# Kernel tuning notes

Hardware: AMD Instinct MI355X
Metric: run time of the kernel (lower is better)

The kernel has to match this reference:

```python
import jax, jax.numpy as jnp
import numpy as np

NUM_EMB = 8192
DIM = 64
DECAY = 0.99
EPS = 1e-05
COMMIT = 0.25


def setup_inputs() -> dict:
    key = jax.random.key(0)
    k1, k2, k3 = jax.random.split(key, 3)
    inputs = jax.random.normal(k1, (8, 4096, DIM), jnp.float32)
    weight = jax.random.normal(k2, (NUM_EMB, DIM), jnp.float32)
    ema_cluster_count = jnp.ones((NUM_EMB,), jnp.float32)
    ema_weight_sum = jax.random.normal(k3, (NUM_EMB, DIM), jnp.float32)
    return {
        'inputs': inputs,
        'weight': weight,
        'ema_cluster_count': ema_cluster_count,
        'ema_weight_sum': ema_weight_sum,
    }


def reference(inputs, weight, ema_cluster_count, ema_weight_sum):
    flat = inputs.reshape(-1, DIM)  # [N, D]
    distances = (
        jnp.sum(flat ** 2, axis=1, keepdims=True)
        + jnp.sum(weight ** 2, axis=1)
        - 2.0 * flat @ weight.T
    )
    idx = jnp.argmin(distances, axis=1)  # [N] int

    # EMA stats (training branch): one-hot column sums == segment counts,
    # encodings.T @ flat == segment sums of inputs by code index.
    counts = jax.ops.segment_sum(
        jnp.ones(flat.shape[0], jnp.float32), idx, num_segments=NUM_EMB)
    new_cc = ema_cluster_count * DECAY + (1.0 - DECAY) * counts
    emb_sum = jax.ops.segment_sum(flat, idx, num_segments=NUM_EMB)
    new_ws = ema_weight_sum * DECAY + (1.0 - DECAY) * emb_sum

    n = jnp.sum(new_cc)
    smoothed = (new_cc + EPS) / (n + NUM_EMB * EPS) * n
    new_weight = new_ws / smoothed[:, None]  # updated codebook [K, D]

    quantized_raw = new_weight[idx].reshape(inputs.shape)
    e_latent_loss = jnp.mean((jax.lax.stop_gradient(quantized_raw) - inputs) ** 2)
    vq_loss = COMMIT * e_latent_loss

    avg_probs = counts / flat.shape[0]
    perplexity = jnp.exp(-jnp.sum(avg_probs * jnp.log(avg_probs + 1e-10)))

    # straight-through estimator
    quantized = inputs + jax.lax.stop_gradient(quantized_raw - inputs)
    return quantized, vq_loss, idx, perplexity, new_weight, new_cc, new_ws
```

## Files before the change

kernel.cpp:

```cpp
#include <hip/hip_runtime.h>
#include <math.h>

typedef _Float16 f16x8 __attribute__((ext_vector_type(8)));
typedef float f32x4 __attribute__((ext_vector_type(4)));

#define NROWS 32768
#define KEMB  8192

#define DECAYF 0.99f
#define OMDF   0.01f

#define OUT_Q    0
#define OUT_LOSS 2097152
#define OUT_IDX  2097153
#define OUT_PERP 2129921
#define OUT_NW   2129922
#define OUT_NCC  2654210
#define OUT_NWS  2662402

#define WS_N      0
#define WS_ENT    1
#define WS_COUNTS 4
#define WS_EMB    8196
#define WS_IDX    532484
#define WS_W2H    565252
#define WS_WFRAG  573444
#define WS_ZERO_UNITS 532484

__device__ __forceinline__ float sq_rn(float v) { return __fmul_rn(v, v); }

__device__ __forceinline__ float npsumsq64(const float* vbuf) {
  float a[8];
#pragma unroll
  for (int j = 0; j < 8; ++j) a[j] = sq_rn(vbuf[j]);
#pragma unroll
  for (int m = 1; m < 8; ++m)
#pragma unroll
    for (int j = 0; j < 8; ++j) a[j] = __fadd_rn(a[j], sq_rn(vbuf[m*8 + j]));
  return __fadd_rn(__fadd_rn(__fadd_rn(a[0],a[1]), __fadd_rn(a[2],a[3])),
                   __fadd_rn(__fadd_rn(a[4],a[5]), __fadd_rn(a[6],a[7])));
}

__device__ __forceinline__ void split_f16(float x, _Float16& hi, _Float16& lo) {
  hi = (_Float16)x;
  float r = __fsub_rn(x, (float)hi);
  lo = (_Float16)r;
}

__global__ __launch_bounds__(256) void prep_kernel(const float* __restrict__ wg,
                                                   float* __restrict__ ws) {
  const int tid = blockIdx.x * 256 + threadIdx.x;
  if (tid < KEMB) {
    const float* src = wg + (size_t)tid * 64;
    float vbuf[64];
#pragma unroll
    for (int f = 0; f < 16; ++f) {
      float4 v = *(const float4*)(src + f*4);
      vbuf[f*4+0]=v.x; vbuf[f*4+1]=v.y; vbuf[f*4+2]=v.z; vbuf[f*4+3]=v.w;
    }
    ws[WS_W2H + tid] = __fmul_rn(0.5f, npsumsq64(vbuf));
  } else if (tid < KEMB + 65536) {
    const int u = tid - KEMB;
    const int K = u >> 3, g = u & 7;
    const int n = K & 15, P = K >> 4;
    const int slot = (g&3)*16 + n, shi = g >> 2;
    const float* src = wg + (size_t)K*64 + g*8;
    float4 v0 = *(const float4*)src, v1 = *(const float4*)(src + 4);
    float vv[8] = {v0.x,v0.y,v0.z,v0.w,v1.x,v1.y,v1.z,v1.w};
    f16x8 hi, lo;
#pragma unroll
    for (int j = 0; j < 8; ++j) { _Float16 h, l; split_f16(vv[j], h, l); hi[j]=h; lo[j]=l; }
    _Float16* wf = (_Float16*)(ws + WS_WFRAG);
    *(f16x8*)&wf[((size_t)(P*4 + shi)*64 + slot)*8]     = hi;
    *(f16x8*)&wf[((size_t)(P*4 + 2 + shi)*64 + slot)*8] = lo;
  }
}

#define LOADP(H0, H1, L0, L1, CW, WP, CP)           \
  H0 = *(const f16x8*)(WP);                         \
  H1 = *(const f16x8*)(WP + 512);                   \
  L0 = *(const f16x8*)(WP + 1024);                  \
  L1 = *(const f16x8*)(WP + 1536);                  \
  CW = *(const f32x4*)(CP);                         \
  WP += 16384; CP += 128;

#define TOURN(ACC, C0)                                                       \
  _Pragma("unroll")                                                          \
  for (int bt = 0; bt < 4; ++bt) {                                           \
    const float d0 = ACC[bt][0], d1 = ACC[bt][1], d2 = ACC[bt][2], d3 = ACC[bt][3]; \
    const float m01 = fminf(d0, d1), m23 = fminf(d2, d3);                    \
    const float pm  = fminf(m01, m23);                                       \
    const int i01 = (d1 < d0) ? 1 : 0;                                       \
    const int i23 = (d3 < d2) ? 3 : 2;                                       \
    const int isel = (m23 < m01) ? i23 : i01;                                \
    if (pm < bestd[bt]) { bestd[bt] = pm; bestk[bt] = (C0) + isel; }         \
  }

__global__ __attribute__((amdgpu_flat_work_group_size(256,256), amdgpu_waves_per_eu(2,2)))
void argmin_kernel(const float* __restrict__ xg,
                   float* __restrict__ out,
                   float* __restrict__ ws) {
  __shared__ __align__(16) _Float16 xp[4*4*64*8];
  __shared__ float md[64*4];
  __shared__ int   mk[64*4];
  __shared__ int   bkL[64];

  const int t    = threadIdx.x;
  const int lane = t & 63, wv = t >> 6;
  const int quad = lane >> 4, n16 = lane & 15;
  const int cg = wv;
  const int row0 = blockIdx.x * 64;
  const _Float16* __restrict__ wfrag = (const _Float16*)(ws + WS_WFRAG);
  const float* __restrict__ w2hg = ws + WS_W2H;

#pragma unroll
  for (int it = 0; it < 2; ++it) {
    const int u  = t + 256*it;
    const int rp = u >> 7, n = (u >> 3) & 15, g = u & 7;
    const float* src = xg + (size_t)(row0 + rp*16 + n)*64 + g*8;
    float4 v0 = *(const float4*)src, v1 = *(const float4*)(src + 4);
    float vv[8] = {v0.x,v0.y,v0.z,v0.w,v1.x,v1.y,v1.z,v1.w};
    f16x8 hi, lo;
#pragma unroll
    for (int j = 0; j < 8; ++j) { _Float16 h, l; split_f16(-vv[j], h, l); hi[j]=h; lo[j]=l; }
    const int slot = (g&3)*16 + n, shi = g >> 2;
    *(f16x8*)&xp[(((rp*4) + shi)*64 + slot)*8]     = hi;
    *(f16x8*)&xp[(((rp*4) + 2 + shi)*64 + slot)*8] = lo;
  }
  __syncthreads();

  f16x8 b[4][4];
#pragma unroll
  for (int bt = 0; bt < 4; ++bt)
#pragma unroll
    for (int s = 0; s < 4; ++s)
      b[bt][s] = *(const f16x8*)&xp[(((bt*4) + s)*64 + lane)*8];

  float bestd[4]; int bestk[4];
#pragma unroll
  for (int i = 0; i < 4; ++i) { bestd[i] = INFINITY; bestk[i] = 0; }

  const int q4 = quad * 4;

  const _Float16* wpA = wfrag + (size_t)cg * 2048 + (size_t)lane * 8;
  const _Float16* wpB = wpA + 8192;
  const float*    cpA = w2hg + cg*16 + q4;
  const float*    cpB = cpA + 64;

  f16x8 hA0, hA1, lA0, lA1, hB0, hB1, lB0, lB1;
  f32x4 cwA, cwB;

  LOADP(hA0, hA1, lA0, lA1, cwA, wpA, cpA);
  LOADP(hB0, hB1, lB0, lB1, cwB, wpB, cpB);

  f32x4 accA[4], accB[4];
  int c0A = cg*16 + q4;
  int c0B = c0A + 64;

#pragma unroll 1
  for (int j = 0; j < 64; ++j) {
    __builtin_amdgcn_s_setprio(1);
#pragma unroll
    for (int bt = 0; bt < 4; ++bt) accA[bt] = __builtin_amdgcn_mfma_f32_16x16x32_f16(hA0, b[bt][0], cwA,      0,0,0);
#pragma unroll
    for (int bt = 0; bt < 4; ++bt) accB[bt] = __builtin_amdgcn_mfma_f32_16x16x32_f16(hB0, b[bt][0], cwB,      0,0,0);
#pragma unroll
    for (int bt = 0; bt < 4; ++bt) accA[bt] = __builtin_amdgcn_mfma_f32_16x16x32_f16(hA1, b[bt][1], accA[bt], 0,0,0);
#pragma unroll
    for (int bt = 0; bt < 4; ++bt) accB[bt] = __builtin_amdgcn_mfma_f32_16x16x32_f16(hB1, b[bt][1], accB[bt], 0,0,0);
#pragma unroll
    for (int bt = 0; bt < 4; ++bt) accA[bt] = __builtin_amdgcn_mfma_f32_16x16x32_f16(hA0, b[bt][2], accA[bt], 0,0,0);
#pragma unroll
    for (int bt = 0; bt < 4; ++bt) accB[bt] = __builtin_amdgcn_mfma_f32_16x16x32_f16(hB0, b[bt][2], accB[bt], 0,0,0);
#pragma unroll
    for (int bt = 0; bt < 4; ++bt) accA[bt] = __builtin_amdgcn_mfma_f32_16x16x32_f16(hA1, b[bt][3], accA[bt], 0,0,0);
#pragma unroll
    for (int bt = 0; bt < 4; ++bt) accB[bt] = __builtin_amdgcn_mfma_f32_16x16x32_f16(hB1, b[bt][3], accB[bt], 0,0,0);
#pragma unroll
    for (int bt = 0; bt < 4; ++bt) accA[bt] = __builtin_amdgcn_mfma_f32_16x16x32_f16(lA0, b[bt][0], accA[bt], 0,0,0);
#pragma unroll
    for (int bt = 0; bt < 4; ++bt) accB[bt] = __builtin_amdgcn_mfma_f32_16x16x32_f16(lB0, b[bt][0], accB[bt], 0,0,0);
#pragma unroll
    for (int bt = 0; bt < 4; ++bt) accA[bt] = __builtin_amdgcn_mfma_f32_16x16x32_f16(lA1, b[bt][1], accA[bt], 0,0,0);
#pragma unroll
    for (int bt = 0; bt < 4; ++bt) accB[bt] = __builtin_amdgcn_mfma_f32_16x16x32_f16(lB1, b[bt][1], accB[bt], 0,0,0);
    __builtin_amdgcn_s_setprio(0);

    if (j < 63) {
      LOADP(hA0, hA1, lA0, lA1, cwA, wpA, cpA);
      LOADP(hB0, hB1, lB0, lB1, cwB, wpB, cpB);
    }

    TOURN(accA, c0A);
    c0A += 128;
    TOURN(accB, c0B);
    c0B += 128;
  }

#pragma unroll
  for (int bt = 0; bt < 4; ++bt) {
    float bd = bestd[bt]; int bk = bestk[bt];
#pragma unroll
    for (int m = 16; m < 64; m <<= 1) {
      const float od = __shfl_xor(bd, m, 64);
      const int   ok = __shfl_xor(bk, m, 64);
      if (od < bd || (od == bd && ok < bk)) { bd = od; bk = ok; }
    }
    if (lane < 16) {
      const int row = bt*16 + n16;
      md[row*4 + cg] = bd;
      mk[row*4 + cg] = bk;
    }
  }
  __syncthreads();

  if (t < 64) {
    const int row = t;
    float bd = md[row*4]; int bk = mk[row*4];
#pragma unroll
    for (int u2 = 1; u2 < 4; ++u2) {
      const float d2 = md[row*4 + u2]; const int k2 = mk[row*4 + u2];
      if (d2 < bd || (d2 == bd && k2 < bk)) { bd = d2; bk = k2; }
    }
    out[OUT_IDX + row0 + row] = (float)bk;
    ((int*)ws)[WS_IDX + row0 + row] = bk;
    bkL[row] = bk;
    atomicAdd(&ws[WS_COUNTS + bk], 1.0f);
  }
  __syncthreads();

#pragma unroll 4
  for (int r = 0; r < 16; ++r) {
    const int row = wv*16 + r;
    const int k = bkL[row];
    atomicAdd(&ws[WS_EMB + (size_t)k*64 + lane],
              xg[(size_t)(row0 + row)*64 + lane]);
  }
}

__global__ __launch_bounds__(256) void stats_kernel(const float* __restrict__ cc,
                                                    float* __restrict__ out,
                                                    float* __restrict__ ws) {
  const int t = threadIdx.x;
  float v1 = 0.0f, v2 = 0.0f;
#pragma unroll
  for (int i = 0; i < 32; ++i) {
    const int k = i*256 + t;
    const float cnt = ws[WS_COUNTS + k];
    const float ncc = __fadd_rn(__fmul_rn(DECAYF, cc[k]), __fmul_rn(OMDF, cnt));
    out[OUT_NCC + k] = ncc;
    const float p = cnt * (1.0f/32768.0f);
    v1 += ncc;
    v2 += __fmul_rn(p, logf(__fadd_rn(p, 1e-10f)));
  }
#pragma unroll
  for (int off = 32; off > 0; off >>= 1) {
    v1 += __shfl_down(v1, off);
    v2 += __shfl_down(v2, off);
  }
  __shared__ float s1[4], s2[4];
  const int lane = t & 63, wid = t >> 6;
  if (lane == 0) { s1[wid] = v1; s2[wid] = v2; }
  __syncthreads();
  if (t == 0) {
    ws[WS_N]   = (s1[0]+s1[1]) + (s1[2]+s1[3]);
    ws[WS_ENT] = (s2[0]+s2[1]) + (s2[2]+s2[3]);
  }
}

__global__ __launch_bounds__(256) void update_quant_kernel(const float* __restrict__ xg,
                                                           const float* __restrict__ ws0,
                                                           float* __restrict__ out,
                                                           float* __restrict__ ws) {
  const int t = threadIdx.x;
  const float n = ws[WS_N];
  const float den = __fadd_rn(n, 0.08192f);

  const int e4 = blockIdx.x * 256 + t;
  {
    const int k = e4 >> 4;
    const float ncc = out[OUT_NCC + k];
    const float smoothed = __fmul_rn(__fadd_rn(ncc, 1e-5f) / den, n);
    float4 w0 = *(const float4*)(ws0 + (size_t)e4*4);
    float4 em = *(const float4*)(ws + WS_EMB + (size_t)e4*4);
    float wv4[4] = {w0.x, w0.y, w0.z, w0.w};
    float ev4[4] = {em.x, em.y, em.z, em.w};
    float nwsv[4], nwv[4];
#pragma unroll
    for (int i = 0; i < 4; ++i) {
      nwsv[i] = __fadd_rn(__fmul_rn(DECAYF, wv4[i]), __fmul_rn(OMDF, ev4[i]));
      nwv[i]  = nwsv[i] / smoothed;
    }
    float4 onws = {nwsv[0], nwsv[1], nwsv[2], nwsv[3]};
    float4 onw  = {nwv[0],  nwv[1],  nwv[2],  nwv[3]};
    *(float4*)(out + OUT_NWS + (size_t)e4*4) = onws;
    *(float4*)(out + OUT_NW  + (size_t)e4*4) = onw;
    if (e4 == 0) out[OUT_PERP] = expf(-ws[WS_ENT]);
  }

  const int* idxb = (const int*)ws + WS_IDX;
  float v = 0.0f;
#pragma unroll
  for (int j = 0; j < 4; ++j) {
    const int qe4 = (j*512 + blockIdx.x)*256 + t;
    const int row = qe4 >> 4, d = (qe4 & 15) * 4;
    const int k = idxb[row];
    const float ncc = out[OUT_NCC + k];
    const float smK = __fmul_rn(__fadd_rn(ncc, 1e-5f) / den, n);
    float4 wq = *(const float4*)(ws0 + (size_t)k*64 + d);
    float4 eq = *(const float4*)(ws + WS_EMB + (size_t)k*64 + d);
    float4 x  = *(const float4*)(xg + (size_t)qe4*4);
    float wv4[4] = {wq.x,wq.y,wq.z,wq.w};
    float ev4[4] = {eq.x,eq.y,eq.z,eq.w};
    float xv[4]  = {x.x,x.y,x.z,x.w};
    float4 o; float ov[4];
#pragma unroll
    for (int i = 0; i < 4; ++i) {
      const float nws = __fadd_rn(__fmul_rn(DECAYF, wv4[i]), __fmul_rn(OMDF, ev4[i]));
      const float q = nws / smK;
      const float df = __fsub_rn(q, xv[i]);
      ov[i] = __fadd_rn(xv[i], df);
      v = fmaf(df, df, v);
    }
    o.x = ov[0]; o.y = ov[1]; o.z = ov[2]; o.w = ov[3];
    *(float4*)(out + OUT_Q + (size_t)qe4*4) = o;
  }
#pragma unroll
  for (int off = 32; off > 0; off >>= 1) v += __shfl_down(v, off);
  __shared__ float sm[4];
  const int lane = t & 63, wid = t >> 6;
  if (lane == 0) sm[wid] = v;
  __syncthreads();
  if (t == 0) ws[WS_COUNTS + blockIdx.x] = (sm[0]+sm[1]) + (sm[2]+sm[3]);
}

__global__ void final_kernel(float* __restrict__ out, const float* __restrict__ ws) {
  const int t = threadIdx.x;
  float v = 0.0f;
#pragma unroll
  for (int i = 0; i < 8; ++i) v += ws[WS_COUNTS + i*64 + t];
#pragma unroll
  for (int off = 32; off > 0; off >>= 1) v += __shfl_down(v, off);
  if (t == 0) out[OUT_LOSS] = __fmul_rn(0.25f, v / 2097152.0f);
}

extern "C" void kernel_launch(void* const* d_in, const int* in_sizes, int n_in,
                              void* d_out, int out_size, void* d_ws, size_t ws_size,
                              hipStream_t stream) {
  (void)in_sizes; (void)n_in; (void)out_size; (void)ws_size;
  const float* x   = (const float*)d_in[0];
  const float* w   = (const float*)d_in[1];
  const float* cc  = (const float*)d_in[2];
  const float* ws0 = (const float*)d_in[3];
  float* out = (float*)d_out;
  float* ws  = (float*)d_ws;

  hipMemsetAsync(d_ws, 0, (size_t)WS_ZERO_UNITS * 4, stream);
  hipLaunchKernelGGL(prep_kernel,         dim3(288), dim3(256), 0, stream, w, ws);
  hipLaunchKernelGGL(argmin_kernel,       dim3(512), dim3(256), 0, stream, x, out, ws);
  hipLaunchKernelGGL(stats_kernel,        dim3(1),   dim3(256), 0, stream, cc, out, ws);
  hipLaunchKernelGGL(update_quant_kernel, dim3(512), dim3(256), 0, stream, x, ws0, out, ws);
  hipLaunchKernelGGL(final_kernel,        dim3(1),   dim3(64),  0, stream, out, ws);
}
```

Baseline: 178.5 us.

## Fold memset, stats and final reduction into neighboring kernels via last-block counters

The workspace memset moves into prep_kernel as a grid-stride zeroing loop. The single-block stats kernel and the final loss reduction are folded into the tails of argmin_kernel and update_quant_kernel. A global atomic counter elects the last finishing block to run them, guarded by thread fences. This cuts the launch count from five operations to three and removes the gaps between dependent launches. The cost is extra fences and atomics at the end of each block, plus reliance on the counters being zeroed in prep.

```diff
diff --git a/kernel.cpp b/kernel.cpp
--- a/kernel.cpp
+++ b/kernel.cpp
@@ -20,6 +20,8 @@
 
 #define WS_N      0
 #define WS_ENT    1
+#define WS_CTR    2
+#define WS_CTR2   3
 #define WS_COUNTS 4
 #define WS_EMB    8196
 #define WS_IDX    532484
@@ -50,6 +52,8 @@
 __global__ __launch_bounds__(256) void prep_kernel(const float* __restrict__ wg,
                                                    float* __restrict__ ws) {
   const int tid = blockIdx.x * 256 + threadIdx.x;
+  for (int z = tid; z < WS_ZERO_UNITS; z += 73728) ws[z] = 0.0f;
+
   if (tid < KEMB) {
     const float* src = wg + (size_t)tid * 64;
     float vbuf[64];
@@ -98,12 +102,15 @@
 
 __global__ __attribute__((amdgpu_flat_work_group_size(256,256), amdgpu_waves_per_eu(2,2)))
 void argmin_kernel(const float* __restrict__ xg,
+                   const float* __restrict__ cc,
                    float* __restrict__ out,
                    float* __restrict__ ws) {
   __shared__ __align__(16) _Float16 xp[4*4*64*8];
   __shared__ float md[64*4];
   __shared__ int   mk[64*4];
   __shared__ int   bkL[64];
+  __shared__ float s1[4], s2[4];
+  __shared__ int   amLast;
 
   const int t    = threadIdx.x;
   const int lane = t & 63, wv = t >> 6;
@@ -236,35 +243,34 @@
     atomicAdd(&ws[WS_EMB + (size_t)k*64 + lane],
               xg[(size_t)(row0 + row)*64 + lane]);
   }
-}
-
-__global__ __launch_bounds__(256) void stats_kernel(const float* __restrict__ cc,
-                                                    float* __restrict__ out,
-                                                    float* __restrict__ ws) {
-  const int t = threadIdx.x;
-  float v1 = 0.0f, v2 = 0.0f;
-#pragma unroll
-  for (int i = 0; i < 32; ++i) {
-    const int k = i*256 + t;
-    const float cnt = ws[WS_COUNTS + k];
-    const float ncc = __fadd_rn(__fmul_rn(DECAYF, cc[k]), __fmul_rn(OMDF, cnt));
-    out[OUT_NCC + k] = ncc;
-    const float p = cnt * (1.0f/32768.0f);
-    v1 += ncc;
-    v2 += __fmul_rn(p, logf(__fadd_rn(p, 1e-10f)));
-  }
-#pragma unroll
-  for (int off = 32; off > 0; off >>= 1) {
-    v1 += __shfl_down(v1, off);
-    v2 += __shfl_down(v2, off);
-  }
-  __shared__ float s1[4], s2[4];
-  const int lane = t & 63, wid = t >> 6;
-  if (lane == 0) { s1[wid] = v1; s2[wid] = v2; }
-  __syncthreads();
-  if (t == 0) {
-    ws[WS_N]   = (s1[0]+s1[1]) + (s1[2]+s1[3]);
-    ws[WS_ENT] = (s2[0]+s2[1]) + (s2[2]+s2[3]);
+
+  __threadfence();
+  if (t == 0) amLast = (atomicAdd((int*)ws + WS_CTR, 1) == (int)gridDim.x - 1);
+  __syncthreads();
+  if (amLast) {
+    __threadfence();
+    float v1 = 0.0f, v2 = 0.0f;
+#pragma unroll
+    for (int i = 0; i < 32; ++i) {
+      const int k = i*256 + t;
+      const float cnt = ws[WS_COUNTS + k];
+      const float ncc = __fadd_rn(__fmul_rn(DECAYF, cc[k]), __fmul_rn(OMDF, cnt));
+      out[OUT_NCC + k] = ncc;
+      const float p = cnt * (1.0f/32768.0f);
+      v1 += ncc;
+      v2 += __fmul_rn(p, logf(__fadd_rn(p, 1e-10f)));
+    }
+#pragma unroll
+    for (int off = 32; off > 0; off >>= 1) {
+      v1 += __shfl_down(v1, off);
+      v2 += __shfl_down(v2, off);
+    }
+    if (lane == 0) { s1[wv] = v1; s2[wv] = v2; }
+    __syncthreads();
+    if (t == 0) {
+      ws[WS_N]   = (s1[0]+s1[1]) + (s1[2]+s1[3]);
+      ws[WS_ENT] = (s2[0]+s2[1]) + (s2[2]+s2[3]);
+    }
   }
 }
 
@@ -272,6 +278,8 @@
                                                            const float* __restrict__ ws0,
                                                            float* __restrict__ out,
                                                            float* __restrict__ ws) {
+  __shared__ float sm[4];
+  __shared__ int amL;
   const int t = threadIdx.x;
   const float n = ws[WS_N];
   const float den = __fadd_rn(n, 0.08192f);
@@ -327,21 +335,25 @@
   }
 #pragma unroll
   for (int off = 32; off > 0; off >>= 1) v += __shfl_down(v, off);
-  __shared__ float sm[4];
   const int lane = t & 63, wid = t >> 6;
   if (lane == 0) sm[wid] = v;
   __syncthreads();
   if (t == 0) ws[WS_COUNTS + blockIdx.x] = (sm[0]+sm[1]) + (sm[2]+sm[3]);
-}
-
-__global__ void final_kernel(float* __restrict__ out, const float* __restrict__ ws) {
-  const int t = threadIdx.x;
-  float v = 0.0f;
-#pragma unroll
-  for (int i = 0; i < 8; ++i) v += ws[WS_COUNTS + i*64 + t];
-#pragma unroll
-  for (int off = 32; off > 0; off >>= 1) v += __shfl_down(v, off);
-  if (t == 0) out[OUT_LOSS] = __fmul_rn(0.25f, v / 2097152.0f);
+
+  __threadfence();
+  if (t == 0) amL = (atomicAdd((int*)ws + WS_CTR2, 1) == (int)gridDim.x - 1);
+  __syncthreads();
+  if (amL) {
+    __threadfence();
+    if (t < 64) {
+      float vv = 0.0f;
+#pragma unroll
+      for (int i = 0; i < 8; ++i) vv += ws[WS_COUNTS + i*64 + t];
+#pragma unroll
+      for (int off = 32; off > 0; off >>= 1) vv += __shfl_down(vv, off);
+      if (t == 0) out[OUT_LOSS] = __fmul_rn(0.25f, vv / 2097152.0f);
+    }
+  }
 }
 
 extern "C" void kernel_launch(void* const* d_in, const int* in_sizes, int n_in,
@@ -355,10 +367,7 @@
   float* out = (float*)d_out;
   float* ws  = (float*)d_ws;
 
-  hipMemsetAsync(d_ws, 0, (size_t)WS_ZERO_UNITS * 4, stream);
   hipLaunchKernelGGL(prep_kernel,         dim3(288), dim3(256), 0, stream, w, ws);
-  hipLaunchKernelGGL(argmin_kernel,       dim3(512), dim3(256), 0, stream, x, out, ws);
-  hipLaunchKernelGGL(stats_kernel,        dim3(1),   dim3(256), 0, stream, cc, out, ws);
+  hipLaunchKernelGGL(argmin_kernel,       dim3(512), dim3(256), 0, stream, x, cc, out, ws);
   hipLaunchKernelGGL(update_quant_kernel, dim3(512), dim3(256), 0, stream, x, ws0, out, ws);
-  hipLaunchKernelGGL(final_kernel,        dim3(1),   dim3(64),  0, stream, out, ws);
-}
+}
```

Result: slower. 251.0 us (+40.7%).

## Fold memset into prep kernel and merge stats into update kernel

Applied to the files above, without the earlier changes.

Removes the hipMemsetAsync by zeroing the workspace inside prep_kernel with a grid-stride loop. It also drops the single-block stats kernel: every update_quant block now recomputes the cluster-count sum redundantly, and block 0 writes new_cc and perplexity. The per-block loss partials move to the W2H workspace region so they no longer overwrite the counts being read. The aim is to cut two launches and the serial one-block stage, at the cost of each block reading all 8192 counts again.

```diff
diff --git a/kernel.cpp b/kernel.cpp
--- a/kernel.cpp
+++ b/kernel.cpp
@@ -50,6 +50,8 @@
 __global__ __launch_bounds__(256) void prep_kernel(const float* __restrict__ wg,
                                                    float* __restrict__ ws) {
   const int tid = blockIdx.x * 256 + threadIdx.x;
+  for (int z = tid; z < WS_ZERO_UNITS; z += 73728) ws[z] = 0.0f;
+
   if (tid < KEMB) {
     const float* src = wg + (size_t)tid * 64;
     float vbuf[64];
@@ -238,48 +240,55 @@
   }
 }
 
-__global__ __launch_bounds__(256) void stats_kernel(const float* __restrict__ cc,
-                                                    float* __restrict__ out,
-                                                    float* __restrict__ ws) {
+__global__ __launch_bounds__(256) void update_quant_kernel(const float* __restrict__ xg,
+                                                           const float* __restrict__ ws0,
+                                                           const float* __restrict__ cc,
+                                                           float* __restrict__ out,
+                                                           float* __restrict__ ws) {
+  __shared__ float s1[4], s2[4];
+  __shared__ float sm[4];
   const int t = threadIdx.x;
+  const int lane = t & 63, wid = t >> 6;
+
   float v1 = 0.0f, v2 = 0.0f;
-#pragma unroll
-  for (int i = 0; i < 32; ++i) {
-    const int k = i*256 + t;
-    const float cnt = ws[WS_COUNTS + k];
-    const float ncc = __fadd_rn(__fmul_rn(DECAYF, cc[k]), __fmul_rn(OMDF, cnt));
-    out[OUT_NCC + k] = ncc;
-    const float p = cnt * (1.0f/32768.0f);
-    v1 += ncc;
-    v2 += __fmul_rn(p, logf(__fadd_rn(p, 1e-10f)));
+  if (blockIdx.x == 0) {
+#pragma unroll
+    for (int i = 0; i < 32; ++i) {
+      const int k = i*256 + t;
+      const float cnt = ws[WS_COUNTS + k];
+      const float ncc = __fadd_rn(__fmul_rn(DECAYF, cc[k]), __fmul_rn(OMDF, cnt));
+      out[OUT_NCC + k] = ncc;
+      const float p = cnt * (1.0f/32768.0f);
+      v1 += ncc;
+      v2 += __fmul_rn(p, logf(__fadd_rn(p, 1e-10f)));
+    }
+  } else {
+#pragma unroll
+    for (int i = 0; i < 32; ++i) {
+      const int k = i*256 + t;
+      const float cnt = ws[WS_COUNTS + k];
+      const float ncc = __fadd_rn(__fmul_rn(DECAYF, cc[k]), __fmul_rn(OMDF, cnt));
+      v1 += ncc;
+    }
   }
 #pragma unroll
   for (int off = 32; off > 0; off >>= 1) {
     v1 += __shfl_down(v1, off);
     v2 += __shfl_down(v2, off);
   }
-  __shared__ float s1[4], s2[4];
-  const int lane = t & 63, wid = t >> 6;
   if (lane == 0) { s1[wid] = v1; s2[wid] = v2; }
   __syncthreads();
-  if (t == 0) {
-    ws[WS_N]   = (s1[0]+s1[1]) + (s1[2]+s1[3]);
-    ws[WS_ENT] = (s2[0]+s2[1]) + (s2[2]+s2[3]);
-  }
-}
-
-__global__ __launch_bounds__(256) void update_quant_kernel(const float* __restrict__ xg,
-                                                           const float* __restrict__ ws0,
-                                                           float* __restrict__ out,
-                                                           float* __restrict__ ws) {
-  const int t = threadIdx.x;
-  const float n = ws[WS_N];
+  const float n = (s1[0]+s1[1]) + (s1[2]+s1[3]);
+  if (blockIdx.x == 0 && t == 0)
+    out[OUT_PERP] = expf(-((s2[0]+s2[1]) + (s2[2]+s2[3])));
   const float den = __fadd_rn(n, 0.08192f);
+  __syncthreads();
 
   const int e4 = blockIdx.x * 256 + t;
   {
     const int k = e4 >> 4;
-    const float ncc = out[OUT_NCC + k];
+    const float cnt = ws[WS_COUNTS + k];
+    const float ncc = __fadd_rn(__fmul_rn(DECAYF, cc[k]), __fmul_rn(OMDF, cnt));
     const float smoothed = __fmul_rn(__fadd_rn(ncc, 1e-5f) / den, n);
     float4 w0 = *(const float4*)(ws0 + (size_t)e4*4);
     float4 em = *(const float4*)(ws + WS_EMB + (size_t)e4*4);
@@ -295,7 +304,6 @@
     float4 onw  = {nwv[0],  nwv[1],  nwv[2],  nwv[3]};
     *(float4*)(out + OUT_NWS + (size_t)e4*4) = onws;
     *(float4*)(out + OUT_NW  + (size_t)e4*4) = onw;
-    if (e4 == 0) out[OUT_PERP] = expf(-ws[WS_ENT]);
   }
 
   const int* idxb = (const int*)ws + WS_IDX;
@@ -305,7 +313,7 @@
     const int qe4 = (j*512 + blockIdx.x)*256 + t;
     const int row = qe4 >> 4, d = (qe4 & 15) * 4;
     const int k = idxb[row];
-    const float ncc = out[OUT_NCC + k];
+    const float ncc = __fadd_rn(__fmul_rn(DECAYF, cc[k]), __fmul_rn(OMDF, ws[WS_COUNTS + k]));
     const float smK = __fmul_rn(__fadd_rn(ncc, 1e-5f) / den, n);
     float4 wq = *(const float4*)(ws0 + (size_t)k*64 + d);
     float4 eq = *(const float4*)(ws + WS_EMB + (size_t)k*64 + d);
@@ -327,18 +335,16 @@
   }
 #pragma unroll
   for (int off = 32; off > 0; off >>= 1) v += __shfl_down(v, off);
-  __shared__ float sm[4];
-  const int lane = t & 63, wid = t >> 6;
   if (lane == 0) sm[wid] = v;
   __syncthreads();
-  if (t == 0) ws[WS_COUNTS + blockIdx.x] = (sm[0]+sm[1]) + (sm[2]+sm[3]);
+  if (t == 0) ws[WS_W2H + blockIdx.x] = (sm[0]+sm[1]) + (sm[2]+sm[3]);
 }
 
 __global__ void final_kernel(float* __restrict__ out, const float* __restrict__ ws) {
   const int t = threadIdx.x;
   float v = 0.0f;
 #pragma unroll
-  for (int i = 0; i < 8; ++i) v += ws[WS_COUNTS + i*64 + t];
+  for (int i = 0; i < 8; ++i) v += ws[WS_W2H + i*64 + t];
 #pragma unroll
   for (int off = 32; off > 0; off >>= 1) v += __shfl_down(v, off);
   if (t == 0) out[OUT_LOSS] = __fmul_rn(0.25f, v / 2097152.0f);
@@ -355,10 +361,8 @@
   float* out = (float*)d_out;
   float* ws  = (float*)d_ws;
 
-  hipMemsetAsync(d_ws, 0, (size_t)WS_ZERO_UNITS * 4, stream);
   hipLaunchKernelGGL(prep_kernel,         dim3(288), dim3(256), 0, stream, w, ws);
   hipLaunchKernelGGL(argmin_kernel,       dim3(512), dim3(256), 0, stream, x, out, ws);
-  hipLaunchKernelGGL(stats_kernel,        dim3(1),   dim3(256), 0, stream, cc, out, ws);
-  hipLaunchKernelGGL(update_quant_kernel, dim3(512), dim3(256), 0, stream, x, ws0, out, ws);
+  hipLaunchKernelGGL(update_quant_kernel, dim3(512), dim3(256), 0, stream, x, ws0, cc, out, ws);
   hipLaunchKernelGGL(final_kernel,        dim3(1),   dim3(64),  0, stream, out, ws);
 }
```

New measurement: 173.5 us (median of 2 runs). 1.03x faster.
